# Optimization experiments

Hardware: AMD Instinct MI355X
Metric: run time of the kernel (lower is better)

The kernel has to match this reference:

```python
import jax, jax.numpy as jnp
import numpy as np
from jax import lax

B, C_IN, T, H = 256, 12, 2048, 128

def lstm_layer(x, W_ih, W_hh, b_ih, b_hh):
    """x: [B,T,in]. PyTorch gate order i,f,g,o. Returns (y [B,T,H], h_T [B,H])."""
    Bb = x.shape[0]
    Hh = W_hh.shape[1]
    # precompute input projections for all timesteps: [B,T,4H]
    xW = jnp.einsum('bti,gi->btg', x, W_ih) + (b_ih + b_hh)
    Whh_T = W_hh.T  # [H,4H]

    def step(carry, xw_t):
        h, c = carry
        g = xw_t + h @ Whh_T                      # [B,4H]
        i, f, gg, o = jnp.split(g, 4, axis=-1)
        i = jax.nn.sigmoid(i)
        f = jax.nn.sigmoid(f)
        gg = jnp.tanh(gg)
        o = jax.nn.sigmoid(o)
        c = f * c + i * gg
        h = o * jnp.tanh(c)
        return (h, c), h

    h0 = jnp.zeros((Bb, Hh), x.dtype)
    c0 = jnp.zeros((Bb, Hh), x.dtype)
    (hT, _), ys = lax.scan(step, (h0, c0), jnp.swapaxes(xW, 0, 1))
    return jnp.swapaxes(ys, 0, 1), hT


def setup_inputs() -> dict:
    key = jax.random.key(0)
    ks = jax.random.split(key, 12)
    s = lambda fan: 1.0 / np.sqrt(fan)
    inp = {
        'x': jax.random.normal(ks[0], (B, C_IN, T), jnp.float32),
        'seq_lengths': jax.random.randint(ks[1], (B,), 1, T + 1),
        # layer 0: input_dim=12 -> H
        'W_ih0': jax.random.normal(ks[2], (4 * H, C_IN), jnp.float32) * s(C_IN),
        'W_hh0': jax.random.normal(ks[3], (4 * H, H), jnp.float32) * s(H),
        'b_ih0': jnp.zeros((4 * H,), jnp.float32),
        'b_hh0': jnp.zeros((4 * H,), jnp.float32),
        # layer 1: H -> H
        'W_ih1': jax.random.normal(ks[4], (4 * H, H), jnp.float32) * s(H),
        'W_hh1': jax.random.normal(ks[5], (4 * H, H), jnp.float32) * s(H),
        'b_ih1': jnp.zeros((4 * H,), jnp.float32),
        'b_hh1': jnp.zeros((4 * H,), jnp.float32),
        # dense head
        'W_dense': jax.random.normal(ks[6], (1, H), jnp.float32) * s(H),
        'b_dense': jnp.zeros((1,), jnp.float32),
    }
    return inp


def reference(x, seq_lengths, W_ih0, W_hh0, b_ih0, b_hh0,
              W_ih1, W_hh1, b_ih1, b_hh1, W_dense, b_dense):
    # x: [B, C, T] -> [B, T, C] (permute(0,2,1))
    x = jnp.transpose(x, (0, 2, 1))
    y, _ = lstm_layer(x, W_ih0, W_hh0, b_ih0, b_hh0)
    _, hT = lstm_layer(y, W_ih1, W_hh1, b_ih1, b_hh1)
    feats = hT                                   # ht.squeeze(): [B,H]
    out = feats @ W_dense.T + b_dense            # [B,1]
    scores = jax.nn.sigmoid(out)
    return scores, feats
```

## Files before the change

### kernel.cpp

```cpp
#include <hip/hip_runtime.h>


typedef short bf16x8 __attribute__((ext_vector_type(8)));
typedef float f32x4 __attribute__((ext_vector_type(4)));
typedef unsigned long long ull;

static constexpr int CIN = 12, T = 2048, H = 128;
static constexpr int NTHR = 512;
static constexpr float L2E = 1.4426950408889634f;

static constexpr int LW1 = 0;
static constexpr int LH0 = 131072;
static constexpr int LH1 = 139264;
static constexpr int LX  = 147456;
static constexpr int LB1 = 149504;
static constexpr int LRED= 151552;
static constexpr int LDS_SZ = 153600;

#if __has_builtin(__builtin_amdgcn_exp2f)
#define EXP2(x) __builtin_amdgcn_exp2f(x)
#else
#define EXP2(x) exp2f(x)
#endif

__device__ __forceinline__ unsigned f2bf(float f) {
  unsigned u = __builtin_bit_cast(unsigned, f);
  return (u + 0x7FFFu + ((u >> 16) & 1u)) >> 16;
}

__device__ __forceinline__ unsigned cvtpk_bf16(float lo, float hi) {
  unsigned r;
  asm("v_cvt_pk_bf16_f32 %0, %1, %2" : "=v"(r) : "v"(lo), "v"(hi));
  return r;
}

__device__ __forceinline__ float sig_pre(float a) {
  return __builtin_amdgcn_rcpf(1.f + EXP2(a));
}

__global__ __launch_bounds__(NTHR, 2) void lstm_merged(
    const float* __restrict__ xg,
    const float* __restrict__ Wih0, const float* __restrict__ Whh0,
    const float* __restrict__ bih0, const float* __restrict__ bhh0,
    const float* __restrict__ Wih1, const float* __restrict__ Whh1,
    const float* __restrict__ bih1, const float* __restrict__ bhh1,
    const float* __restrict__ Wd,   const float* __restrict__ bd,
    float* __restrict__ out)
{
  __shared__ char lds[LDS_SZ];
  const int tid = threadIdx.x;
  const int l  = tid & 63;
  const int w  = tid >> 6;
  const int lg = l >> 4;
  const int lr = l & 15;
  const int b0 = blockIdx.x * 16;

  for (int i = tid; i < 18432 / 4; i += NTHR) ((int*)(lds + LH0))[i] = 0;
  {
    const float4* Wv = (const float4*)Wih1;
    #pragma unroll 4
    for (int i = 0; i < 32; ++i) {
      const int idx = i * 512 + tid;
      const float4 f = Wv[idx];
      const int e0 = idx * 4;
      const int n = e0 >> 7, k = e0 & 127;
      const int tau = n >> 4;
      const float s = ((tau >> 3) == 2) ? (2.f * L2E) : (-L2E);
      const int lane = ((k >> 3) & 3) * 16 + (n & 15);
      const int byte = ((tau * 4 + (k >> 5)) * 64 + lane) * 16 + (k & 7) * 2;
      const unsigned lo = cvtpk_bf16(f.x * s, f.y * s);
      const unsigned hi = cvtpk_bf16(f.z * s, f.w * s);
      *(ull*)(lds + LW1 + byte) = ((ull)hi << 32) | lo;
    }
  }
  {
    const float s = ((tid >> 7) == 2) ? (2.f * L2E) : (-L2E);
    ((float*)(lds + LB1))[tid] = (bih1[tid] + bhh1[tid]) * s;
  }
  __syncthreads();
  if (tid < 32) {
    const int buf = tid >> 4, b = tid & 15;
    *(unsigned short*)(lds + LX + buf * 1024 + 256 + b * 16 + 8) = 0x3F80;
  }

  bf16x8 A0[4][5];
  bf16x8 A1h[4][4];
  #pragma unroll
  for (int q = 0; q < 4; ++q) {
    const int n = (q * 8 + w) * 16 + lr;
    const float s = (q == 2) ? (2.f * L2E) : (-L2E);
    #pragma unroll
    for (int kf = 0; kf < 4; ++kf) {
      const float* s0 = &Whh0[n * H + kf * 32 + lg * 8];
      const float* s1 = &Whh1[n * H + kf * 32 + lg * 8];
      #pragma unroll
      for (int j = 0; j < 8; ++j) {
        A0[q][kf][j]  = (short)f2bf(s0[j] * s);
        A1h[q][kf][j] = (short)f2bf(s1[j] * s);
      }
    }
    #pragma unroll
    for (int j = 0; j < 8; ++j) {
      const int k = lg * 8 + j;
      float v = 0.f;
      if (k < CIN) v = Wih0[n * CIN + k] * s;
      else if (k == CIN) v = (bih0[n] + bhh0[n]) * s;
      A0[q][4][j] = (short)f2bf(v);
    }
  }
  const f32x4 zed = {0.f, 0.f, 0.f, 0.f};

  const int rdB  = lg * 256 + lr * 16;
  const int bcol = w * 16 + lg * 4;
  const int wrH  = (bcol >> 3) * 256 + lr * 16 + (bcol & 7) * 2;
  const int bq   = (w * 16 + lg * 4) * 4;
  const int xb = tid & 15, xc = tid >> 4;
  const int wrX = (xc >> 3) * 256 + xb * 16 + (xc & 7) * 2;
  const size_t xbase = (size_t)(b0 + xb) * (CIN * T) + (size_t)xc * T;

  if (tid < 192)
    *(unsigned short*)(lds + LX + wrX) = (unsigned short)f2bf(xg[xbase]);
  __syncthreads();

  float c0v[4] = {0.f, 0.f, 0.f, 0.f};
  float c1v[4] = {0.f, 0.f, 0.f, 0.f};
  float h1v[4] = {0.f, 0.f, 0.f, 0.f};

  #pragma unroll 2
  for (int t = 0; t < T; ++t) {
    const int p = t & 1;
    float xnext = 0.f;
    if (tid < 192) xnext = xg[xbase + (t + 1 < T ? t + 1 : t)];

    bf16x8 bfH0[4], bfH1[4], bfX;
    #pragma unroll
    for (int kf = 0; kf < 4; ++kf) {
      bfH0[kf] = *(const bf16x8*)(lds + LH0 + (1 - p) * 4096 + kf * 1024 + rdB);
      bfH1[kf] = *(const bf16x8*)(lds + LH1 + p * 4096 + kf * 1024 + rdB);
    }
    bfX = *(const bf16x8*)(lds + LX + p * 1024 + rdB);

    f32x4 accA[4], accB[4];
    #pragma unroll
    for (int q = 0; q < 4; ++q) {
      accA[q] = zed;
      accB[q] = *(const f32x4*)(lds + LB1 + bq + q * 512);
    }
    #pragma unroll
    for (int kf = 0; kf < 4; ++kf) {
      bf16x8 af[4];
      #pragma unroll
      for (int q = 0; q < 4; ++q)
        af[q] = *(const bf16x8*)(lds + LW1 + ((q * 8 + w) * 4 + kf) * 1024 + l * 16);
      #pragma unroll
      for (int q = 0; q < 4; ++q) {
        accA[q] = __builtin_amdgcn_mfma_f32_16x16x32_bf16(A0[q][kf],  bfH0[kf], accA[q], 0, 0, 0);
        accB[q] = __builtin_amdgcn_mfma_f32_16x16x32_bf16(A1h[q][kf], bfH1[kf], accB[q], 0, 0, 0);
        accB[q] = __builtin_amdgcn_mfma_f32_16x16x32_bf16(af[q],      bfH0[kf], accB[q], 0, 0, 0);
      }
    }
    #pragma unroll
    for (int q = 0; q < 4; ++q)
      accA[q] = __builtin_amdgcn_mfma_f32_16x16x32_bf16(A0[q][4], bfX, accA[q], 0, 0, 0);

    {
      float h0t[4];
      #pragma unroll
      for (int r = 0; r < 4; ++r) {
        const float iv = sig_pre(accA[0][r]);
        const float fv = sig_pre(accA[1][r]);
        const float gv = fmaf(-2.f, sig_pre(accA[2][r]), 1.f);
        const float ov = sig_pre(accA[3][r]);
        const float c  = fmaf(fv, c0v[r], iv * gv);
        c0v[r] = c;
        const float th = fmaf(-2.f, sig_pre(c * (2.f * L2E)), 1.f);
        h0t[r] = ov * th;
      }
      const unsigned hp0 = cvtpk_bf16(h0t[0], h0t[1]);
      const unsigned hp1 = cvtpk_bf16(h0t[2], h0t[3]);
      *(ull*)(lds + LH0 + p * 4096 + wrH) = ((ull)hp1 << 32) | hp0;
    }
    if (t > 0) {
      #pragma unroll
      for (int r = 0; r < 4; ++r) {
        const float iv = sig_pre(accB[0][r]);
        const float fv = sig_pre(accB[1][r]);
        const float gv = fmaf(-2.f, sig_pre(accB[2][r]), 1.f);
        const float ov = sig_pre(accB[3][r]);
        const float c  = fmaf(fv, c1v[r], iv * gv);
        c1v[r] = c;
        const float th = fmaf(-2.f, sig_pre(c * (2.f * L2E)), 1.f);
        h1v[r] = ov * th;
      }
      const unsigned hp0 = cvtpk_bf16(h1v[0], h1v[1]);
      const unsigned hp1 = cvtpk_bf16(h1v[2], h1v[3]);
      *(ull*)(lds + LH1 + (1 - p) * 4096 + wrH) = ((ull)hp1 << 32) | hp0;
    }
    if (tid < 192) {
      *(unsigned short*)(lds + LX + (1 - p) * 1024 + wrX) =
          (unsigned short)cvtpk_bf16(xnext, xnext);
    }
    __syncthreads();
  }

  {
    bf16x8 bfH0[4], bfH1[4];
    #pragma unroll
    for (int kf = 0; kf < 4; ++kf) {
      bfH0[kf] = *(const bf16x8*)(lds + LH0 + 4096 + kf * 1024 + rdB);
      bfH1[kf] = *(const bf16x8*)(lds + LH1 + kf * 1024 + rdB);
    }
    f32x4 accB[4];
    #pragma unroll
    for (int q = 0; q < 4; ++q)
      accB[q] = *(const f32x4*)(lds + LB1 + bq + q * 512);
    #pragma unroll
    for (int kf = 0; kf < 4; ++kf) {
      bf16x8 af[4];
      #pragma unroll
      for (int q = 0; q < 4; ++q)
        af[q] = *(const bf16x8*)(lds + LW1 + ((q * 8 + w) * 4 + kf) * 1024 + l * 16);
      #pragma unroll
      for (int q = 0; q < 4; ++q) {
        accB[q] = __builtin_amdgcn_mfma_f32_16x16x32_bf16(A1h[q][kf], bfH1[kf], accB[q], 0, 0, 0);
        accB[q] = __builtin_amdgcn_mfma_f32_16x16x32_bf16(af[q],      bfH0[kf], accB[q], 0, 0, 0);
      }
    }
    #pragma unroll
    for (int r = 0; r < 4; ++r) {
      const float iv = sig_pre(accB[0][r]);
      const float fv = sig_pre(accB[1][r]);
      const float gv = fmaf(-2.f, sig_pre(accB[2][r]), 1.f);
      const float ov = sig_pre(accB[3][r]);
      const float c  = fmaf(fv, c1v[r], iv * gv);
      c1v[r] = c;
      const float th = fmaf(-2.f, sig_pre(c * (2.f * L2E)), 1.f);
      h1v[r] = ov * th;
    }
  }

  const float4 wd = *(const float4*)&Wd[bcol];
  const float partial = h1v[0] * wd.x + h1v[1] * wd.y + h1v[2] * wd.z + h1v[3] * wd.w;
  #pragma unroll
  for (int r = 0; r < 4; ++r)
    out[256 + (size_t)(b0 + lr) * H + (bcol + r)] = h1v[r];
  ((float*)(lds + LRED))[tid] = partial;
  __syncthreads();
  if (tid < 16) {
    float s = 0.f;
    #pragma unroll 8
    for (int k = 0; k < 32; ++k) s += ((float*)(lds + LRED))[tid + 16 * k];
    const float v = s + bd[0];
    out[b0 + tid] = __builtin_amdgcn_rcpf(1.f + EXP2(-v * L2E));
  }
}

extern "C" void kernel_launch(void* const* d_in, const int* in_sizes, int n_in,
                              void* d_out, int out_size, void* d_ws, size_t ws_size,
                              hipStream_t stream) {
  const float* x    = (const float*)d_in[0];
  const float* Wih0 = (const float*)d_in[2];
  const float* Whh0 = (const float*)d_in[3];
  const float* bih0 = (const float*)d_in[4];
  const float* bhh0 = (const float*)d_in[5];
  const float* Wih1 = (const float*)d_in[6];
  const float* Whh1 = (const float*)d_in[7];
  const float* bih1 = (const float*)d_in[8];
  const float* bhh1 = (const float*)d_in[9];
  const float* Wd   = (const float*)d_in[10];
  const float* bd   = (const float*)d_in[11];
  (void)in_sizes; (void)n_in; (void)out_size; (void)d_ws; (void)ws_size;

  lstm_merged<<<dim3(16), dim3(NTHR), 0, stream>>>(
      x, Wih0, Whh0, bih0, bhh0, Wih1, Whh1, bih1, bhh1, Wd, bd, (float*)d_out);
}
```

Baseline: 3.597 ms.

## Split layer-0 and layer-1 MFMA chains and software-pipeline W_ih1 LDS loads

```diff
diff --git a/kernel.cpp b/kernel.cpp
--- a/kernel.cpp
+++ b/kernel.cpp
@@ -126,6 +126,11 @@
   float c1v[4] = {0.f, 0.f, 0.f, 0.f};
   float h1v[4] = {0.f, 0.f, 0.f, 0.f};
 
+  bf16x8 afc[4], afn[4];
+  #pragma unroll
+  for (int q = 0; q < 4; ++q)
+    afc[q] = *(const bf16x8*)(lds + LW1 + ((q * 8 + w) * 4 + 0) * 1024 + l * 16);
+
   #pragma unroll 2
   for (int t = 0; t < T; ++t) {
     const int p = t & 1;
@@ -140,28 +145,15 @@
     }
     bfX = *(const bf16x8*)(lds + LX + p * 1024 + rdB);
 
-    f32x4 accA[4], accB[4];
-    #pragma unroll
-    for (int q = 0; q < 4; ++q) {
-      accA[q] = zed;
-      accB[q] = *(const f32x4*)(lds + LB1 + bq + q * 512);
-    }
-    #pragma unroll
-    for (int kf = 0; kf < 4; ++kf) {
-      bf16x8 af[4];
+    f32x4 accA[4];
+    #pragma unroll
+    for (int q = 0; q < 4; ++q)
+      accA[q] = __builtin_amdgcn_mfma_f32_16x16x32_bf16(A0[q][4], bfX, zed, 0, 0, 0);
+    #pragma unroll
+    for (int kf = 0; kf < 4; ++kf)
       #pragma unroll
       for (int q = 0; q < 4; ++q)
-        af[q] = *(const bf16x8*)(lds + LW1 + ((q * 8 + w) * 4 + kf) * 1024 + l * 16);
-      #pragma unroll
-      for (int q = 0; q < 4; ++q) {
-        accA[q] = __builtin_amdgcn_mfma_f32_16x16x32_bf16(A0[q][kf],  bfH0[kf], accA[q], 0, 0, 0);
-        accB[q] = __builtin_amdgcn_mfma_f32_16x16x32_bf16(A1h[q][kf], bfH1[kf], accB[q], 0, 0, 0);
-        accB[q] = __builtin_amdgcn_mfma_f32_16x16x32_bf16(af[q],      bfH0[kf], accB[q], 0, 0, 0);
-      }
-    }
-    #pragma unroll
-    for (int q = 0; q < 4; ++q)
-      accA[q] = __builtin_amdgcn_mfma_f32_16x16x32_bf16(A0[q][4], bfX, accA[q], 0, 0, 0);
+        accA[q] = __builtin_amdgcn_mfma_f32_16x16x32_bf16(A0[q][kf], bfH0[kf], accA[q], 0, 0, 0);
 
     {
       float h0t[4];
@@ -180,6 +172,29 @@
       const unsigned hp1 = cvtpk_bf16(h0t[2], h0t[3]);
       *(ull*)(lds + LH0 + p * 4096 + wrH) = ((ull)hp1 << 32) | hp0;
     }
+
+    f32x4 accB[4];
+    #pragma unroll
+    for (int q = 0; q < 4; ++q)
+      accB[q] = *(const f32x4*)(lds + LB1 + bq + q * 512);
+    #pragma unroll
+    for (int kf = 0; kf < 4; ++kf) {
+      if (kf < 3) {
+        #pragma unroll
+        for (int q = 0; q < 4; ++q)
+          afn[q] = *(const bf16x8*)(lds + LW1 + ((q * 8 + w) * 4 + kf + 1) * 1024 + l * 16);
+      }
+      #pragma unroll
+      for (int q = 0; q < 4; ++q) {
+        accB[q] = __builtin_amdgcn_mfma_f32_16x16x32_bf16(A1h[q][kf], bfH1[kf], accB[q], 0, 0, 0);
+        accB[q] = __builtin_amdgcn_mfma_f32_16x16x32_bf16(afc[q],     bfH0[kf], accB[q], 0, 0, 0);
+      }
+      if (kf < 3) {
+        #pragma unroll
+        for (int q = 0; q < 4; ++q) afc[q] = afn[q];
+      }
+    }
+
     if (t > 0) {
       #pragma unroll
       for (int r = 0; r < 4; ++r) {
@@ -200,6 +215,9 @@
       *(unsigned short*)(lds + LX + (1 - p) * 1024 + wrX) =
           (unsigned short)cvtpk_bf16(xnext, xnext);
     }
+    #pragma unroll
+    for (int q = 0; q < 4; ++q)
+      afc[q] = *(const bf16x8*)(lds + LW1 + ((q * 8 + w) * 4 + 0) * 1024 + l * 16);
     __syncthreads();
   }
 
@@ -216,14 +234,19 @@
       accB[q] = *(const f32x4*)(lds + LB1 + bq + q * 512);
     #pragma unroll
     for (int kf = 0; kf < 4; ++kf) {
-      bf16x8 af[4];
-      #pragma unroll
-      for (int q = 0; q < 4; ++q)
-        af[q] = *(const bf16x8*)(lds + LW1 + ((q * 8 + w) * 4 + kf) * 1024 + l * 16);
+      if (kf < 3) {
+        #pragma unroll
+        for (int q = 0; q < 4; ++q)
+          afn[q] = *(const bf16x8*)(lds + LW1 + ((q * 8 + w) * 4 + kf + 1) * 1024 + l * 16);
+      }
       #pragma unroll
       for (int q = 0; q < 4; ++q) {
         accB[q] = __builtin_amdgcn_mfma_f32_16x16x32_bf16(A1h[q][kf], bfH1[kf], accB[q], 0, 0, 0);
-        accB[q] = __builtin_amdgcn_mfma_f32_16x16x32_bf16(af[q],      bfH0[kf], accB[q], 0, 0, 0);
+        accB[q] = __builtin_amdgcn_mfma_f32_16x16x32_bf16(afc[q],     bfH0[kf], accB[q], 0, 0, 0);
+      }
+      if (kf < 3) {
+        #pragma unroll
+        for (int q = 0; q < 4; ++q) afc[q] = afn[q];
       }
     }
     #pragma unroll
```

Measured after the change: 3.447 ms. 4.2% less time.
